# Kernel tuning notes

Measured on AMD Instinct MI355X. Metric: run time of the kernel, lower is better.

## Reference

```python
import jax, jax.numpy as jnp
import numpy as np
from jax import lax


def setup_inputs() -> dict:
    key = jax.random.key(0)
    k1, k2 = jax.random.split(key)
    L, B, D = 1024, 16, 1024
    x = jax.random.normal(k1, (L, B, D), dtype=jnp.float32)
    # weight maps n_in -> n_out*k with k=3 (n_in == n_out); small scale for stability
    weight = jax.random.normal(k2, (D, 3 * D), dtype=jnp.float32) * 0.05
    bias = jnp.zeros((2 * D,), dtype=jnp.float32)
    c0 = jnp.zeros((B, D), dtype=jnp.float32)
    return {"x": x, "weight": weight, "bias": bias, "c0": c0}


def reference(x, weight, bias, c0):
    # SRUCell forward, k == 3 (n_in == n_out), unidirectional, tanh activation,
    # no dropout masks (mask_h == NULL -> mask = 1).
    L, B, D = x.shape
    u = (x.reshape(L * B, D) @ weight).reshape(L, B, D, 3)
    b1 = bias[:D]
    b2 = bias[D:]
    u0 = u[..., 0]                                   # [L, B, D]
    g1 = jax.nn.sigmoid(u[..., 1] + b1)              # forget gate
    g2 = jax.nn.sigmoid(u[..., 2] + b2)              # reset/highway gate

    def step(c, inp):
        u0_t, g1_t, g2_t, x_t = inp
        c_new = (c - u0_t) * g1_t + u0_t             # c = c'*g1 + u0*(1-g1)
        h_t = (jnp.tanh(c_new) - x_t) * g2_t + x_t   # h = act(c)*g2 + x*(1-g2)
        return c_new, h_t

    c_last, h = lax.scan(step, c0, (u0, g1, g2, x))
    return h, c_last
```

## Files before the change

### kernel.cpp

```cpp
#include <hip/hip_runtime.h>

#define L_DIM 1024
#define B_DIM 16
#define D_DIM 1024
#define K_DIM 1024
#define N_DIM 3072
#define M_DIM (L_DIM * B_DIM)
#define CHAINS 16384
#define CHUNK 32
#define NCHUNK 32

typedef float f32x4 __attribute__((ext_vector_type(4)));
typedef __bf16 bf16x8 __attribute__((ext_vector_type(8)));
typedef unsigned short u16;
typedef unsigned int u32;

__device__ __forceinline__ u16 f2bf(float f) {
  u32 u = __float_as_uint(f);
  u = u + 0x7FFFu + ((u >> 16) & 1u);
  return (u16)(u >> 16);
}
__device__ __forceinline__ float bf2f(u16 v) {
  return __uint_as_float(((u32)v) << 16);
}
__device__ __forceinline__ float bf2f_lo(u32 v) {
  return __uint_as_float(v << 16);
}
__device__ __forceinline__ float bf2f_hi(u32 v) {
  return __uint_as_float(v & 0xffff0000u);
}
__device__ __forceinline__ float fexp(float v) {
  return __builtin_amdgcn_exp2f(v * 1.4426950408889634f);
}
__device__ __forceinline__ float sigm(float z) {
  return __builtin_amdgcn_rcpf(1.0f + fexp(-z));
}
__device__ __forceinline__ float ftanh(float v) {
  return 1.0f - 2.0f * __builtin_amdgcn_rcpf(1.0f + fexp(2.0f * v));
}

__global__ __launch_bounds__(256) void cvt_x_kernel(const float4* __restrict__ in,
                                                    ushort4* __restrict__ out, int n4) {
  int i = blockIdx.x * 256 + threadIdx.x;
  if (i < n4) {
    float4 v = in[i];
    ushort4 o;
    o.x = f2bf(v.x); o.y = f2bf(v.y); o.z = f2bf(v.z); o.w = f2bf(v.w);
    out[i] = o;
  }
}

__global__ __launch_bounds__(256) void cvt_w_kernel(const float* __restrict__ W,
                                                    u16* __restrict__ Wt) {
  __shared__ float tile[64][65];
  int c0 = blockIdx.x * 64;
  int r0 = blockIdx.y * 64;
  int tx = threadIdx.x & 63;
  int ty = threadIdx.x >> 6;
#pragma unroll
  for (int i = 0; i < 16; ++i) {
    int row = i * 4 + ty;
    tile[row][tx] = W[(size_t)(r0 + row) * N_DIM + c0 + tx];
  }
  __syncthreads();
#pragma unroll
  for (int i = 0; i < 16; ++i) {
    int crow = i * 4 + ty;
    int c = c0 + crow;
    int nprime = (c % 3) * D_DIM + (c / 3);
    Wt[(size_t)nprime * K_DIM + r0 + tx] = f2bf(tile[tx][crow]);
  }
}


#define AS1 __attribute__((address_space(1)))
#define AS3 __attribute__((address_space(3)))
#define STAGE(gp, lp) do { \
  __builtin_amdgcn_global_load_lds((const AS1 void*)(gp), (AS3 void*)(lp), 16, 0, 0); \
  __builtin_amdgcn_global_load_lds((const AS1 void*)((gp) + (size_t)64 * K_DIM), \
                                   (AS3 void*)((lp) + 4096), 16, 0, 0); \
} while (0)

#define QUAD(AI, JB, BF) \
  _Pragma("unroll") \
  for (int i = 0; i < 4; ++i) { \
    _Pragma("unroll") \
    for (int j = 0; j < 2; ++j) { \
      acc[AI + i][JB + j] = __builtin_amdgcn_mfma_f32_16x16x32_bf16(aF[i][0], BF[j][0], acc[AI + i][JB + j], 0, 0, 0); \
      acc[AI + i][JB + j] = __builtin_amdgcn_mfma_f32_16x16x32_bf16(aF[i][1], BF[j][1], acc[AI + i][JB + j], 0, 0, 0); \
    } \
  }

__global__ __launch_bounds__(512, 2) void gemm_kernel(const u16* __restrict__ A,
                                                      const u16* __restrict__ Bt,
                                                      u16* __restrict__ U) {
  __shared__ __align__(16) u16 sm[65536];
  const int tid = threadIdx.x;
  const int wave = tid >> 6;
  const int lane = tid & 63;
  const int wm = wave >> 2;
  const int wn = wave & 3;
  const int quad = lane >> 4;
  const int l16 = lane & 15;

  const int flat = blockIdx.y * 12 + blockIdx.x;
  const int swz = (flat & 7) * 96 + (flat >> 3);
  const int m0 = (swz / 12) * 256;
  const int n0 = (swz % 12) * 256;

  const int rr = tid >> 3;
  const int slot = (tid & 7) ^ (rr & 7);
  const u16* gA = A + (size_t)(m0 + rr) * K_DIM + slot * 8;
  const u16* gB = Bt + (size_t)(n0 + rr) * K_DIM + slot * 8;

  u16* ldsA = sm + wave * 512;
  u16* ldsB = sm + 32768 + wave * 512;

  const int swzu = (l16 & 7) << 3;
  const int c0 = (quad * 8) ^ swzu;
  const int c1 = (32 + quad * 8) ^ swzu;
  const u16* pA = sm + (wm * 128 + l16) * 64;
  const u16* pB = sm + 32768 + (wn * 64 + l16) * 64;

  f32x4 acc[8][4] = {};

  STAGE(gA, ldsA);
  STAGE(gA + (size_t)128 * K_DIM, ldsA + 8192);
  STAGE(gB, ldsB);
  STAGE(gB + (size_t)128 * K_DIM, ldsB + 8192);
  STAGE(gB + 64, ldsB + 16384);
  STAGE(gB + (size_t)128 * K_DIM + 64, ldsB + 16384 + 8192);
  asm volatile("s_waitcnt vmcnt(0)" ::: "memory");
  __builtin_amdgcn_s_barrier();

  for (int u = 0; u < 16; ++u) {
    const int buf = u & 1;
    const int nb = buf ^ 1;
    const u16* pAb = pA + buf * 16384;
    const u16* pBb = pB + buf * 16384;
    bf16x8 aF[4][2], bLo[2][2], bHi[2][2];

#pragma unroll
    for (int i = 0; i < 4; ++i) {
      aF[i][0] = *(const bf16x8*)(pAb + i * 1024 + c0);
      aF[i][1] = *(const bf16x8*)(pAb + i * 1024 + c1);
    }
#pragma unroll
    for (int j = 0; j < 2; ++j) {
      bLo[j][0] = *(const bf16x8*)(pBb + j * 1024 + c0);
      bLo[j][1] = *(const bf16x8*)(pBb + j * 1024 + c1);
    }
    if (u < 15) STAGE(gA + (u + 1) * 64, ldsA + nb * 16384);
    __builtin_amdgcn_s_barrier();
    __builtin_amdgcn_s_setprio(1);
    QUAD(0, 0, bLo)
    __builtin_amdgcn_s_setprio(0);
    __builtin_amdgcn_s_barrier();

#pragma unroll
    for (int j = 0; j < 2; ++j) {
      bHi[j][0] = *(const bf16x8*)(pBb + (2 + j) * 1024 + c0);
      bHi[j][1] = *(const bf16x8*)(pBb + (2 + j) * 1024 + c1);
    }
    if (u < 15) STAGE(gA + (size_t)128 * K_DIM + (u + 1) * 64, ldsA + nb * 16384 + 8192);
    __builtin_amdgcn_s_barrier();
    __builtin_amdgcn_s_setprio(1);
    QUAD(0, 2, bHi)
    __builtin_amdgcn_s_setprio(0);
    __builtin_amdgcn_s_barrier();

#pragma unroll
    for (int i = 0; i < 4; ++i) {
      aF[i][0] = *(const bf16x8*)(pAb + (4 + i) * 1024 + c0);
      aF[i][1] = *(const bf16x8*)(pAb + (4 + i) * 1024 + c1);
    }
    if (u < 14) STAGE(gB + (u + 2) * 64, ldsB + buf * 16384);
    __builtin_amdgcn_s_barrier();
    __builtin_amdgcn_s_setprio(1);
    QUAD(4, 2, bHi)
    __builtin_amdgcn_s_setprio(0);
    __builtin_amdgcn_s_barrier();

    if (u < 14) {
      STAGE(gB + (size_t)128 * K_DIM + (u + 2) * 64, ldsB + buf * 16384 + 8192);
      asm volatile("s_waitcnt vmcnt(4)" ::: "memory");
    } else if (u == 14) {
      asm volatile("s_waitcnt vmcnt(0)" ::: "memory");
    }
    __builtin_amdgcn_s_barrier();
    __builtin_amdgcn_s_setprio(1);
    QUAD(4, 0, bLo)
    __builtin_amdgcn_s_setprio(0);
    __builtin_amdgcn_s_barrier();
  }

#pragma unroll
  for (int i = 0; i < 8; ++i) {
#pragma unroll
    for (int j = 0; j < 4; ++j) {
      const int col = n0 + wn * 64 + j * 16 + l16;
      const int rb = m0 + wm * 128 + i * 16 + quad * 4;
#pragma unroll
      for (int r = 0; r < 4; ++r)
        U[(size_t)(rb + r) * N_DIM + col] = f2bf(acc[i][j][r]);
    }
  }
}


__global__ __launch_bounds__(256) void sru_phase1(const u16* __restrict__ U,
                                                  const float* __restrict__ bias,
                                                  float* __restrict__ Aarr,
                                                  float* __restrict__ Barr) {
  int tid = blockIdx.x * 256 + threadIdx.x;
  int pair = tid & (CHAINS / 2 - 1);
  int j = tid >> 13;
  int d2 = (pair & 511) << 1;
  int b = pair >> 9;
  float2 bb1 = *(const float2*)(bias + d2);
  const u16* p = U + (size_t)(j * CHUNK * B_DIM + b) * N_DIM + d2;
  float A0 = 1.0f, B0 = 0.0f, A1 = 1.0f, B1 = 0.0f;
#pragma unroll 4
  for (int s = 0; s < CHUNK; ++s) {
    u32 w0 = *(const u32*)p;
    u32 w1 = *(const u32*)(p + D_DIM);
    float u0a = bf2f_lo(w0), u0b = bf2f_hi(w0);
    float g1a = sigm(bf2f_lo(w1) + bb1.x);
    float g1b = sigm(bf2f_hi(w1) + bb1.y);
    B0 = (B0 - u0a) * g1a + u0a;
    B1 = (B1 - u0b) * g1b + u0b;
    A0 *= g1a;
    A1 *= g1b;
    p += (size_t)B_DIM * N_DIM;
  }
  int chain0 = b * D_DIM + d2;
  *(float2*)(Aarr + (size_t)j * CHAINS + chain0) = make_float2(A0, A1);
  *(float2*)(Barr + (size_t)j * CHAINS + chain0) = make_float2(B0, B1);
}

__global__ __launch_bounds__(256) void sru_phase2(const float* __restrict__ Aarr,
                                                  const float* __restrict__ Barr,
                                                  const float* __restrict__ c0,
                                                  float* __restrict__ Cin,
                                                  float* __restrict__ clast) {
  int chain = blockIdx.x * 256 + threadIdx.x;
  float As[NCHUNK], Bs[NCHUNK];
#pragma unroll
  for (int j = 0; j < NCHUNK; ++j) {
    As[j] = Aarr[(size_t)j * CHAINS + chain];
    Bs[j] = Barr[(size_t)j * CHAINS + chain];
  }
  float c = c0[chain];
#pragma unroll
  for (int j = 0; j < NCHUNK; ++j) {
    Cin[(size_t)j * CHAINS + chain] = c;
    c = As[j] * c + Bs[j];
  }
  clast[chain] = c;
}

__global__ __launch_bounds__(256) void sru_phase3(const u16* __restrict__ U,
                                                  const float* __restrict__ x,
                                                  const float* __restrict__ bias,
                                                  const float* __restrict__ Cin,
                                                  float* __restrict__ h) {
  int tid = blockIdx.x * 256 + threadIdx.x;
  int pair = tid & (CHAINS / 2 - 1);
  int j = tid >> 13;
  int d2 = (pair & 511) << 1;
  int b = pair >> 9;
  float2 bb1 = *(const float2*)(bias + d2);
  float2 bb2 = *(const float2*)(bias + D_DIM + d2);
  int chain0 = b * D_DIM + d2;
  float2 c = *(const float2*)(Cin + (size_t)j * CHAINS + chain0);
  size_t m0 = (size_t)(j * CHUNK * B_DIM + b);
  const u16* p = U + m0 * N_DIM + d2;
  const float* xp = x + m0 * D_DIM + d2;
  float* hp = h + m0 * D_DIM + d2;
#pragma unroll 4
  for (int s = 0; s < CHUNK; ++s) {
    u32 w0 = *(const u32*)p;
    u32 w1 = *(const u32*)(p + D_DIM);
    u32 w2 = *(const u32*)(p + 2 * D_DIM);
    float2 xv = *(const float2*)xp;
    float u0a = bf2f_lo(w0), u0b = bf2f_hi(w0);
    float g1a = sigm(bf2f_lo(w1) + bb1.x);
    float g1b = sigm(bf2f_hi(w1) + bb1.y);
    float g2a = sigm(bf2f_lo(w2) + bb2.x);
    float g2b = sigm(bf2f_hi(w2) + bb2.y);
    c.x = (c.x - u0a) * g1a + u0a;
    c.y = (c.y - u0b) * g1b + u0b;
    float2 hv;
    hv.x = (ftanh(c.x) - xv.x) * g2a + xv.x;
    hv.y = (ftanh(c.y) - xv.y) * g2b + xv.y;
    *(float2*)hp = hv;
    p += (size_t)B_DIM * N_DIM;
    xp += B_DIM * D_DIM;
    hp += B_DIM * D_DIM;
  }
}

extern "C" void kernel_launch(void* const* d_in, const int* in_sizes, int n_in,
                              void* d_out, int out_size, void* d_ws, size_t ws_size,
                              hipStream_t stream) {
  const float* x = (const float*)d_in[0];
  const float* W = (const float*)d_in[1];
  const float* bias = (const float*)d_in[2];
  const float* c0 = (const float*)d_in[3];
  float* out = (float*)d_out;

  char* ws = (char*)d_ws;
  u16* xb = (u16*)ws;
  u16* wt = (u16*)(ws + 33554432);
  u16* U = (u16*)(ws + 33554432 + 6291456);
  float* Aarr = (float*)ws;
  float* Barr = (float*)(ws + 2097152);
  float* Cin  = (float*)(ws + 4194304);

  cvt_x_kernel<<<16384, 256, 0, stream>>>((const float4*)x, (ushort4*)xb, M_DIM * K_DIM / 4);
  cvt_w_kernel<<<dim3(48, 16), 256, 0, stream>>>(W, wt);
  gemm_kernel<<<dim3(N_DIM / 256, M_DIM / 256), 512, 0, stream>>>(xb, wt, U);
  sru_phase1<<<CHAINS / 2 * NCHUNK / 256, 256, 0, stream>>>(U, bias, Aarr, Barr);
  sru_phase2<<<CHAINS / 256, 256, 0, stream>>>(Aarr, Barr, c0, Cin, out + (size_t)M_DIM * D_DIM);
  sru_phase3<<<CHAINS / 2 * NCHUNK / 256, 256, 0, stream>>>(U, x, bias, Cin, out);
}
```

Baseline: 279.8 us.

## Fuse three-phase chunked SRU scan into one kernel with shared-memory carry

Replaces the three scan kernels (per-chunk A/B reduction, carry propagation, final recompute) with one kernel. Each 512-thread block owns 32 chains across all 32 chunks, keeps A/B/carry in LDS, and syncs within the block instead of across kernel launches. This removes two launches and the global round trips for A, B and Cin. The trade-off is a grid of only 512 blocks, and a serial carry step where just 32 threads are active while the rest wait at the barrier, which may lower occupancy and latency hiding. A block-index swizzle spreads neighbouring blocks across batch rows.

```diff
diff --git a/kernel.cpp b/kernel.cpp
--- a/kernel.cpp
+++ b/kernel.cpp
@@ -208,95 +208,88 @@
 }
 
 
-__global__ __launch_bounds__(256) void sru_phase1(const u16* __restrict__ U,
-                                                  const float* __restrict__ bias,
-                                                  float* __restrict__ Aarr,
-                                                  float* __restrict__ Barr) {
-  int tid = blockIdx.x * 256 + threadIdx.x;
-  int pair = tid & (CHAINS / 2 - 1);
-  int j = tid >> 13;
-  int d2 = (pair & 511) << 1;
-  int b = pair >> 9;
-  float2 bb1 = *(const float2*)(bias + d2);
-  const u16* p = U + (size_t)(j * CHUNK * B_DIM + b) * N_DIM + d2;
-  float A0 = 1.0f, B0 = 0.0f, A1 = 1.0f, B1 = 0.0f;
+__global__ __launch_bounds__(512) void sru_fused(const u16* __restrict__ U,
+                                                 const float* __restrict__ x,
+                                                 const float* __restrict__ bias,
+                                                 const float* __restrict__ c0,
+                                                 float* __restrict__ h,
+                                                 float* __restrict__ clast) {
+  __shared__ float sA[NCHUNK][32];
+  __shared__ float sB[NCHUNK][32];
+  __shared__ float sC[NCHUNK][32];
+
+  const int flat = blockIdx.x;
+  const int cb = (flat & 7) * 64 + (flat >> 3);
+  const int b  = cb >> 5;
+  const int d0 = (cb & 31) << 5;
+  const int t  = threadIdx.x;
+  const int pr = t & 15;
+  const int j  = t >> 4;
+  const int d2 = d0 + pr * 2;
+
+  const float2 bb1 = *(const float2*)(bias + d2);
+
+  {
+    const u16* p = U + (size_t)(j * CHUNK * B_DIM + b) * N_DIM + d2;
+    float A0 = 1.0f, A1 = 1.0f, B0 = 0.0f, B1 = 0.0f;
 #pragma unroll 4
-  for (int s = 0; s < CHUNK; ++s) {
-    u32 w0 = *(const u32*)p;
-    u32 w1 = *(const u32*)(p + D_DIM);
-    float u0a = bf2f_lo(w0), u0b = bf2f_hi(w0);
-    float g1a = sigm(bf2f_lo(w1) + bb1.x);
-    float g1b = sigm(bf2f_hi(w1) + bb1.y);
-    B0 = (B0 - u0a) * g1a + u0a;
-    B1 = (B1 - u0b) * g1b + u0b;
-    A0 *= g1a;
-    A1 *= g1b;
-    p += (size_t)B_DIM * N_DIM;
-  }
-  int chain0 = b * D_DIM + d2;
-  *(float2*)(Aarr + (size_t)j * CHAINS + chain0) = make_float2(A0, A1);
-  *(float2*)(Barr + (size_t)j * CHAINS + chain0) = make_float2(B0, B1);
-}
-
-__global__ __launch_bounds__(256) void sru_phase2(const float* __restrict__ Aarr,
-                                                  const float* __restrict__ Barr,
-                                                  const float* __restrict__ c0,
-                                                  float* __restrict__ Cin,
-                                                  float* __restrict__ clast) {
-  int chain = blockIdx.x * 256 + threadIdx.x;
-  float As[NCHUNK], Bs[NCHUNK];
-#pragma unroll
-  for (int j = 0; j < NCHUNK; ++j) {
-    As[j] = Aarr[(size_t)j * CHAINS + chain];
-    Bs[j] = Barr[(size_t)j * CHAINS + chain];
-  }
-  float c = c0[chain];
-#pragma unroll
-  for (int j = 0; j < NCHUNK; ++j) {
-    Cin[(size_t)j * CHAINS + chain] = c;
-    c = As[j] * c + Bs[j];
-  }
-  clast[chain] = c;
-}
-
-__global__ __launch_bounds__(256) void sru_phase3(const u16* __restrict__ U,
-                                                  const float* __restrict__ x,
-                                                  const float* __restrict__ bias,
-                                                  const float* __restrict__ Cin,
-                                                  float* __restrict__ h) {
-  int tid = blockIdx.x * 256 + threadIdx.x;
-  int pair = tid & (CHAINS / 2 - 1);
-  int j = tid >> 13;
-  int d2 = (pair & 511) << 1;
-  int b = pair >> 9;
-  float2 bb1 = *(const float2*)(bias + d2);
-  float2 bb2 = *(const float2*)(bias + D_DIM + d2);
-  int chain0 = b * D_DIM + d2;
-  float2 c = *(const float2*)(Cin + (size_t)j * CHAINS + chain0);
-  size_t m0 = (size_t)(j * CHUNK * B_DIM + b);
-  const u16* p = U + m0 * N_DIM + d2;
-  const float* xp = x + m0 * D_DIM + d2;
-  float* hp = h + m0 * D_DIM + d2;
+    for (int s = 0; s < CHUNK; ++s) {
+      u32 w0 = *(const u32*)p;
+      u32 w1 = *(const u32*)(p + D_DIM);
+      float u0a = bf2f_lo(w0), u0b = bf2f_hi(w0);
+      float g1a = sigm(bf2f_lo(w1) + bb1.x);
+      float g1b = sigm(bf2f_hi(w1) + bb1.y);
+      B0 = (B0 - u0a) * g1a + u0a;
+      B1 = (B1 - u0b) * g1b + u0b;
+      A0 *= g1a;
+      A1 *= g1b;
+      p += (size_t)B_DIM * N_DIM;
+    }
+    *(float2*)&sA[j][pr * 2] = make_float2(A0, A1);
+    *(float2*)&sB[j][pr * 2] = make_float2(B0, B1);
+  }
+  __syncthreads();
+
+  if (t < 32) {
+    const int chain = cb * 32 + t;
+    float c = c0[chain];
+#pragma unroll
+    for (int jj = 0; jj < NCHUNK; ++jj) {
+      sC[jj][t] = c;
+      c = sA[jj][t] * c + sB[jj][t];
+    }
+    clast[chain] = c;
+  }
+  __syncthreads();
+
+  {
+    const float2 bb2 = *(const float2*)(bias + D_DIM + d2);
+    float2 c = *(const float2*)&sC[j][pr * 2];
+    const size_t m0 = (size_t)(j * CHUNK * B_DIM + b);
+    const u16* p = U + m0 * N_DIM + d2;
+    const float* xp = x + m0 * D_DIM + d2;
+    float* hp = h + m0 * D_DIM + d2;
 #pragma unroll 4
-  for (int s = 0; s < CHUNK; ++s) {
-    u32 w0 = *(const u32*)p;
-    u32 w1 = *(const u32*)(p + D_DIM);
-    u32 w2 = *(const u32*)(p + 2 * D_DIM);
-    float2 xv = *(const float2*)xp;
-    float u0a = bf2f_lo(w0), u0b = bf2f_hi(w0);
-    float g1a = sigm(bf2f_lo(w1) + bb1.x);
-    float g1b = sigm(bf2f_hi(w1) + bb1.y);
-    float g2a = sigm(bf2f_lo(w2) + bb2.x);
-    float g2b = sigm(bf2f_hi(w2) + bb2.y);
-    c.x = (c.x - u0a) * g1a + u0a;
-    c.y = (c.y - u0b) * g1b + u0b;
-    float2 hv;
-    hv.x = (ftanh(c.x) - xv.x) * g2a + xv.x;
-    hv.y = (ftanh(c.y) - xv.y) * g2b + xv.y;
-    *(float2*)hp = hv;
-    p += (size_t)B_DIM * N_DIM;
-    xp += B_DIM * D_DIM;
-    hp += B_DIM * D_DIM;
+    for (int s = 0; s < CHUNK; ++s) {
+      u32 w0 = *(const u32*)p;
+      u32 w1 = *(const u32*)(p + D_DIM);
+      u32 w2 = *(const u32*)(p + 2 * D_DIM);
+      float2 xv = *(const float2*)xp;
+      float u0a = bf2f_lo(w0), u0b = bf2f_hi(w0);
+      float g1a = sigm(bf2f_lo(w1) + bb1.x);
+      float g1b = sigm(bf2f_hi(w1) + bb1.y);
+      float g2a = sigm(bf2f_lo(w2) + bb2.x);
+      float g2b = sigm(bf2f_hi(w2) + bb2.y);
+      c.x = (c.x - u0a) * g1a + u0a;
+      c.y = (c.y - u0b) * g1b + u0b;
+      float2 hv;
+      hv.x = (ftanh(c.x) - xv.x) * g2a + xv.x;
+      hv.y = (ftanh(c.y) - xv.y) * g2b + xv.y;
+      *(float2*)hp = hv;
+      p += (size_t)B_DIM * N_DIM;
+      xp += B_DIM * D_DIM;
+      hp += B_DIM * D_DIM;
+    }
   }
 }
 
@@ -313,14 +306,9 @@
   u16* xb = (u16*)ws;
   u16* wt = (u16*)(ws + 33554432);
   u16* U = (u16*)(ws + 33554432 + 6291456);
-  float* Aarr = (float*)ws;
-  float* Barr = (float*)(ws + 2097152);
-  float* Cin  = (float*)(ws + 4194304);
 
   cvt_x_kernel<<<16384, 256, 0, stream>>>((const float4*)x, (ushort4*)xb, M_DIM * K_DIM / 4);
   cvt_w_kernel<<<dim3(48, 16), 256, 0, stream>>>(W, wt);
   gemm_kernel<<<dim3(N_DIM / 256, M_DIM / 256), 512, 0, stream>>>(xb, wt, U);
-  sru_phase1<<<CHAINS / 2 * NCHUNK / 256, 256, 0, stream>>>(U, bias, Aarr, Barr);
-  sru_phase2<<<CHAINS / 256, 256, 0, stream>>>(Aarr, Barr, c0, Cin, out + (size_t)M_DIM * D_DIM);
-  sru_phase3<<<CHAINS / 2 * NCHUNK / 256, 256, 0, stream>>>(U, x, bias, Cin, out);
-}
+  sru_fused<<<512, 512, 0, stream>>>(U, x, bias, c0, out, out + (size_t)M_DIM * D_DIM);
+}
```

Result: slower. 285.9 us (+2.2%).
